# Optimization experiments

Measured on AMD Instinct MI355X. Metric: run time of the kernel, lower is better.

The kernel has to match this reference:

```python
import jax, jax.numpy as jnp
import numpy as np
from jax import lax

INPUT_DIM = 256
STATE_DIM = 512
B, T = 128, 1024


def setup_inputs() -> dict:
    key = jax.random.key(0)
    ks = jax.random.split(key, 9)
    s = STATE_DIM
    i = INPUT_DIM
    # Linear(state_dim, state_dim, bias=False), weight scaled by 0.2 as in __init__
    lim_s = 1.0 / np.sqrt(s)
    lim_i = 1.0 / np.sqrt(i)
    A0_w = jax.random.uniform(ks[0], (s, s), jnp.float32, -lim_s, lim_s) * 0.2
    A1_w = jax.random.uniform(ks[1], (s, s), jnp.float32, -lim_s, lim_s) * 0.2
    B0_w = jax.random.uniform(ks[2], (s, i), jnp.float32, -lim_i, lim_i)
    B0_b = jax.random.uniform(ks[3], (s,), jnp.float32, -lim_i, lim_i)
    B1_w = jax.random.uniform(ks[4], (s, i), jnp.float32, -lim_i, lim_i)
    B1_b = jax.random.uniform(ks[5], (s,), jnp.float32, -lim_i, lim_i)
    gate_w = jax.random.uniform(ks[6], (s, i), jnp.float32, -lim_i, lim_i)
    gate_b = jax.random.uniform(ks[7], (s,), jnp.float32, -lim_i, lim_i)
    x_seq = jax.random.normal(ks[8], (B, T, i), jnp.float32)
    s0 = jnp.zeros((B, s), jnp.float32)
    alpha = jnp.float32(0.5)
    return {
        "x_seq": x_seq, "s0": s0,
        "A0_w": A0_w, "B0_w": B0_w, "B0_b": B0_b,
        "A1_w": A1_w, "B1_w": B1_w, "B1_b": B1_b,
        "gate_w": gate_w, "gate_b": gate_b,
        "alpha": alpha, "z": 1,
    }


def reference(x_seq, s0, A0_w, B0_w, B0_b, A1_w, B1_w, B1_b, gate_w, gate_b, alpha, z):
    # Precompute all input projections in one batched GEMM each: [B, T, S]
    bx0 = jnp.einsum('bti,si->bts', x_seq, B0_w) + B0_b
    bx1 = jnp.einsum('bti,si->bts', x_seq, B1_w) + B1_b
    gx = jax.nn.sigmoid(jnp.einsum('bti,si->bts', x_seq, gate_w) + gate_b)

    def step_fn(s, inputs):
        b0_t, b1_t, g_t = inputs  # each [B, S]
        f0 = jnp.tanh(s @ A0_w.T + b0_t)
        if z == 0:
            f = f0
        else:
            f1 = jnp.tanh(s @ A1_w.T + b1_t)
            f = (1.0 - alpha) * f0 + alpha * f1
        s_new = g_t * f + (1.0 - g_t) * s
        return s_new, s_new

    # scan over time: move T to leading axis
    xs = (jnp.swapaxes(bx0, 0, 1), jnp.swapaxes(bx1, 0, 1), jnp.swapaxes(gx, 0, 1))
    _, states = lax.scan(step_fn, s0, xs)  # states: [T, B, S]
    # prepend s0 -> [B, T+1, S]
    return jnp.concatenate([s0[:, None, :], jnp.swapaxes(states, 0, 1)], axis=1)
```

## Files before the change

### kernel.cpp

```cpp
#include <hip/hip_runtime.h>
#include <hip/hip_bf16.h>
#include <math.h>

typedef __attribute__((ext_vector_type(8))) short bf16x8;
typedef __attribute__((ext_vector_type(4))) float f32x4;
typedef __attribute__((ext_vector_type(4))) unsigned int u32x4;
typedef __attribute__((ext_vector_type(2))) unsigned int u32x2;

#define TT 1024
#define BB 128
#define II 256
#define SS 512
#define OUT_T 1025
#define OUT_BSTRIDE ((size_t)OUT_T * SS)

static __device__ __forceinline__ unsigned short f2bf(float f) {
  union { float f; unsigned int u; } v; v.f = f;
  unsigned int r = v.u + 0x7fffu + ((v.u >> 16) & 1u);
  return (unsigned short)(r >> 16);
}
static __device__ __forceinline__ float bf2f(unsigned short h) {
  union { unsigned int u; float f; } v; v.u = ((unsigned int)h) << 16;
  return v.f;
}
static __device__ __forceinline__ bf16x8 pack8(const float* p) {
  float4 a = *(const float4*)p;
  float4 b = *(const float4*)(p + 4);
  bf16x8 r;
  r[0]=(short)f2bf(a.x); r[1]=(short)f2bf(a.y); r[2]=(short)f2bf(a.z); r[3]=(short)f2bf(a.w);
  r[4]=(short)f2bf(b.x); r[5]=(short)f2bf(b.y); r[6]=(short)f2bf(b.z); r[7]=(short)f2bf(b.w);
  return r;
}
static __device__ __forceinline__ float bfat(u32x2 v, int q) {
  unsigned int u = (q < 2) ? v[0] : v[1];
  u = (q & 1) ? (u >> 16) : (u & 0xffffu);
  return bf2f((unsigned short)u);
}
static __device__ __forceinline__ float fast_tanh(float x) {
  float x2 = fminf(x * 2.8853900817779268f, 88.0f);
  float e = __builtin_amdgcn_exp2f(x2);
  return (e - 1.0f) * __builtin_amdgcn_rcpf(e + 1.0f);
}

static __device__ __forceinline__ void st_coh_b128(void* p, u32x4 v) {
  asm volatile("global_store_dwordx4 %0, %1, off sc0 sc1" :: "v"(p), "v"(v) : "memory");
}

static __device__ __forceinline__ void mega_acquire(const char* an,
    u32x4& v0, u32x4& v1, u32x4& v2, u32x4& v3,
    u32x4& v4, u32x4& v5, u32x4& v6, u32x4& v7) {
  asm volatile(
    "global_load_dwordx4 %0, %8, off sc0 sc1\n\t"
    "global_load_dwordx4 %1, %8, off offset:256 sc0 sc1\n\t"
    "global_load_dwordx4 %2, %8, off offset:512 sc0 sc1\n\t"
    "global_load_dwordx4 %3, %8, off offset:768 sc0 sc1\n\t"
    "global_load_dwordx4 %4, %8, off offset:1024 sc0 sc1\n\t"
    "global_load_dwordx4 %5, %8, off offset:1280 sc0 sc1\n\t"
    "global_load_dwordx4 %6, %8, off offset:1536 sc0 sc1\n\t"
    "global_load_dwordx4 %7, %8, off offset:1792 sc0 sc1\n\t"
    "s_waitcnt vmcnt(0)"
    : "=&v"(v0), "=&v"(v1), "=&v"(v2), "=&v"(v3),
      "=&v"(v4), "=&v"(v5), "=&v"(v6), "=&v"(v7)
    : "v"(an) : "memory");
  __builtin_amdgcn_sched_barrier(0);
}
static __device__ __forceinline__ unsigned chk4(u32x4 v, unsigned expd) {
  return ((((v[0] ^ expd) | (v[1] ^ expd) | (v[2] ^ expd) | (v[3] ^ expd)) & 0xffffu) != 0u) ? 1u : 0u;
}

__global__ __launch_bounds__(256) void proj_kernel(
    const float* __restrict__ x,
    const float* __restrict__ B0w, const float* __restrict__ B0b,
    const float* __restrict__ B1w, const float* __restrict__ B1b,
    const float* __restrict__ Gw,  const float* __restrict__ Gb,
    unsigned short* __restrict__ proj)
{
  __shared__ unsigned short Xs[64 * 264];
  __shared__ unsigned short Ws[64 * 40];

  int m0 = blockIdx.x * 64;
  int tid = threadIdx.x, lane = tid & 63, wid = tid >> 6;
  int lane15 = lane & 15, kslot = lane >> 4;
  int mt0 = (wid >> 1) * 2, nt0 = (wid & 1) * 2;
  int sr = tid >> 2, sc = tid & 3;

#pragma unroll
  for (int it = 0; it < 8; ++it) {
    int task = tid + 256 * it; int r = task >> 5, c = task & 31;
    *(bf16x8*)&Xs[r * 264 + c * 8] = pack8(x + (size_t)(m0 + r) * II + c * 8);
  }
  __syncthreads();

  for (int nt = 0; nt < 24; ++nt) {
    int n0 = nt * 64;
    const float* Wp; const float* bp; bool isgate = false;
    if (n0 < 512)       { Wp = B0w + (size_t)n0 * II;          bp = B0b + n0; }
    else if (n0 < 1024) { Wp = B1w + (size_t)(n0 - 512) * II;  bp = B1b + (n0 - 512); }
    else                { Wp = Gw  + (size_t)(n0 - 1024) * II; bp = Gb + (n0 - 1024); isgate = true; }

    f32x4 acc[2][2] = {};
    for (int k0 = 0; k0 < II; k0 += 32) {
      __syncthreads();
      *(bf16x8*)&Ws[sr * 40 + sc * 8] = pack8(Wp + (size_t)sr * II + k0 + sc * 8);
      __syncthreads();
      bf16x8 af[2], bf[2];
#pragma unroll
      for (int mi = 0; mi < 2; ++mi)
        af[mi] = *(const bf16x8*)&Xs[((mt0 + mi) * 16 + lane15) * 264 + k0 + 8 * kslot];
#pragma unroll
      for (int ni = 0; ni < 2; ++ni)
        bf[ni] = *(const bf16x8*)&Ws[((nt0 + ni) * 16 + lane15) * 40 + 8 * kslot];
#pragma unroll
      for (int mi = 0; mi < 2; ++mi)
#pragma unroll
        for (int ni = 0; ni < 2; ++ni)
          acc[mi][ni] = __builtin_amdgcn_mfma_f32_16x16x32_bf16(af[mi], bf[ni], acc[mi][ni], 0, 0, 0);
    }
#pragma unroll
    for (int mi = 0; mi < 2; ++mi)
#pragma unroll
      for (int ni = 0; ni < 2; ++ni)
#pragma unroll
        for (int q = 0; q < 4; ++q) {
          int m  = m0 + (mt0 + mi) * 16 + kslot * 4 + q;
          int nl = (nt0 + ni) * 16 + lane15;
          int b = m >> 10, t = m & 1023;
          float v = acc[mi][ni][q] + bp[nl];
          if (isgate) v = 1.0f / (1.0f + expf(-v));
          proj[((size_t)t * BB + b) * 1536 + n0 + nl] = f2bf(v);
        }
  }
}

__global__ __launch_bounds__(256, 1) void recur_kernel(
    const float* __restrict__ s0,
    const float* __restrict__ A0w, const float* __restrict__ A1w,
    const unsigned short* __restrict__ proj,
    const float* __restrict__ alpha_p, const int* __restrict__ z_p,
    unsigned int* state32,
    float* __restrict__ out)
{
  __shared__ unsigned short Sbuf[2][16 * 520];

  int tid = threadIdx.x, lane = tid & 63, wid = tid >> 6;
  int g = blockIdx.x & 7, j = blockIdx.x >> 3;
  int b0 = g * 16, c0 = j * 64;
  int lane15 = lane & 15, kslot = lane >> 4;
  int colA = c0 + wid * 16 + lane15;
  int ccb  = c0 + wid * 16 + kslot * 4;
  int row  = b0 + lane15;
  int prow = tid >> 4, pch = tid & 15;
  float alpha = *alpha_p; int z = *z_p; float om_a = 1.0f - alpha;

  bf16x8 Af0[16], Af1[16];
#pragma unroll
  for (int kk = 0; kk < 16; ++kk) {
    int k0 = kk * 32 + kslot * 8;
    Af0[kk] = pack8(A0w + (size_t)colA * SS + k0);
    Af1[kk] = pack8(A1w + (size_t)colA * SS + k0);
  }

#pragma unroll
  for (int c2 = 0; c2 < 4; ++c2) {
    int e = tid + 256 * c2; int rr = e >> 6, kc = e & 63;
    *(bf16x8*)&Sbuf[0][rr * 520 + kc * 8] = pack8(s0 + (size_t)(b0 + rr) * SS + kc * 8);
  }
  if (j == 0) {
#pragma unroll
    for (int it = 0; it < 8; ++it) {
      int task = tid + 256 * it;
      int rr = task >> 7, f4 = task & 127;
      *(float4*)(out + (size_t)(b0 + rr) * OUT_BSTRIDE + f4 * 4) =
          *(const float4*)(s0 + (size_t)(b0 + rr) * SS + f4 * 4);
    }
  }
  float4 sp4 = *(const float4*)(s0 + (size_t)row * SS + ccb);
  float sprev[4] = {sp4.x, sp4.y, sp4.z, sp4.w};

  const unsigned short* pp = proj + (size_t)row * 1536 + ccb;
  u32x2 pb0 = *(const u32x2*)(pp);
  u32x2 pb1 = *(const u32x2*)(pp + 512);
  u32x2 pg  = *(const u32x2*)(pp + 1024);

  unsigned int* pub0 = state32 + (size_t)row * SS + ccb;
  unsigned int* pub1 = pub0 + (size_t)BB * SS;
  const char* acq0 = (const char*)(state32 + (size_t)(b0 + prow) * SS) + pch * 16;
  const char* acq1 = acq0 + (size_t)BB * SS * 4;
  float* outp = out + (size_t)row * OUT_BSTRIDE + ccb;

  __syncthreads();

  for (int t = 0; t < TT; ++t) {
    int par = t & 1;

    if (t > 0) {
      unsigned expd = (unsigned)t;
      const char* acqc = par ? acq1 : acq0;
      u32x4 v0, v1, v2, v3, v4, v5, v6, v7;
      mega_acquire(acqc, v0, v1, v2, v3, v4, v5, v6, v7);
      unsigned own = 1u << j;
      for (;;) {
        unsigned st =
            (chk4(v0, expd) << 0) | (chk4(v1, expd) << 1) |
            (chk4(v2, expd) << 2) | (chk4(v3, expd) << 3) |
            (chk4(v4, expd) << 4) | (chk4(v5, expd) << 5) |
            (chk4(v6, expd) << 6) | (chk4(v7, expd) << 7);
        st &= ~own;
        if (st == 0u) break;
        mega_acquire(acqc, v0, v1, v2, v3, v4, v5, v6, v7);
      }
      unsigned short* sl = &Sbuf[par][prow * 520 + pch * 4];
#define LAND(S, V) if ((S) != j) {                                    \
        unsigned d0 = ((V)[0] >> 16) | ((V)[1] & 0xffff0000u);        \
        unsigned d1 = ((V)[2] >> 16) | ((V)[3] & 0xffff0000u);        \
        u32x2 dd; dd[0] = d0; dd[1] = d1;                             \
        *(u32x2*)(sl + (S) * 64) = dd; }
      LAND(0, v0) LAND(1, v1) LAND(2, v2) LAND(3, v3)
      LAND(4, v4) LAND(5, v5) LAND(6, v6) LAND(7, v7)
#undef LAND
      __syncthreads();
    }

    f32x4 a0e = {}, a0o = {}, a1e = {}, a1o = {};
    const unsigned short* sb = &Sbuf[par][lane15 * 520 + kslot * 8];
#pragma unroll
    for (int kk = 0; kk < 16; kk += 2) {
      bf16x8 f0 = *(const bf16x8*)(sb + kk * 32);
      bf16x8 f1 = *(const bf16x8*)(sb + (kk + 1) * 32);
      a0e = __builtin_amdgcn_mfma_f32_16x16x32_bf16(Af0[kk],     f0, a0e, 0, 0, 0);
      a1e = __builtin_amdgcn_mfma_f32_16x16x32_bf16(Af1[kk],     f0, a1e, 0, 0, 0);
      a0o = __builtin_amdgcn_mfma_f32_16x16x32_bf16(Af0[kk + 1], f1, a0o, 0, 0, 0);
      a1o = __builtin_amdgcn_mfma_f32_16x16x32_bf16(Af1[kk + 1], f1, a1o, 0, 0, 0);
    }

    float sn[4];
#pragma unroll
    for (int q = 0; q < 4; ++q) {
      float f0 = fast_tanh((a0e[q] + a0o[q]) + bfat(pb0, q));
      float f;
      if (z != 0) {
        float f1 = fast_tanh((a1e[q] + a1o[q]) + bfat(pb1, q));
        f = om_a * f0 + alpha * f1;
      } else f = f0;
      float gg = bfat(pg, q);
      sn[q] = gg * f + (1.0f - gg) * sprev[q];
      sprev[q] = sn[q];
    }

    {
      u32x2 dd;
      dd[0] = (unsigned)f2bf(sn[0]) | ((unsigned)f2bf(sn[1]) << 16);
      dd[1] = (unsigned)f2bf(sn[2]) | ((unsigned)f2bf(sn[3]) << 16);
      *(u32x2*)&Sbuf[par ^ 1][lane15 * 520 + ccb] = dd;
    }
    {
      unsigned nxt = (unsigned)(t + 1);
      u32x4 w;
#pragma unroll
      for (int q = 0; q < 4; ++q) w[q] = ((unsigned)f2bf(sn[q]) << 16) | nxt;
      st_coh_b128(par ? pub0 : pub1, w);
    }
    outp += SS;
    {
      float4 o4 = {sn[0], sn[1], sn[2], sn[3]};
      *(float4*)outp = o4;
    }
    if (t + 1 < TT) {
      pp += (size_t)BB * 1536;
      pb0 = *(const u32x2*)(pp);
      pb1 = *(const u32x2*)(pp + 512);
      pg  = *(const u32x2*)(pp + 1024);
    }
  }
}

extern "C" void kernel_launch(void* const* d_in, const int* in_sizes, int n_in,
                              void* d_out, int out_size, void* d_ws, size_t ws_size,
                              hipStream_t stream) {
  const float* x   = (const float*)d_in[0];
  const float* s0  = (const float*)d_in[1];
  const float* A0w = (const float*)d_in[2];
  const float* B0w = (const float*)d_in[3];
  const float* B0b = (const float*)d_in[4];
  const float* A1w = (const float*)d_in[5];
  const float* B1w = (const float*)d_in[6];
  const float* B1b = (const float*)d_in[7];
  const float* Gw  = (const float*)d_in[8];
  const float* Gb  = (const float*)d_in[9];
  const float* alp = (const float*)d_in[10];
  const int*   zp  = (const int*)d_in[11];
  float* out = (float*)d_out;

  char* ws = (char*)d_ws;
  size_t proj_bytes  = (size_t)BB * TT * 1536 * 2;
  size_t state_bytes = (size_t)2 * BB * SS * 4;
  unsigned short* proj    = (unsigned short*)(ws);
  unsigned int*   state32 = (unsigned int*)(ws + proj_bytes);

  hipMemsetAsync(state32, 0, state_bytes, stream);

  proj_kernel<<<dim3(131072 / 64), dim3(256), 0, stream>>>(
      x, B0w, B0b, B1w, B1b, Gw, Gb, proj);

  recur_kernel<<<dim3(64), dim3(256), 0, stream>>>(
      s0, A0w, A1w, proj, alp, zp, state32, out);
}
```

Baseline: 3.031 ms.

## Interleave two batch groups per block to hide inter-block state exchange latency

The recurrence kernel now runs on 32 blocks instead of 64, and each block handles two 16-row batch groups (A and B). Per time step it alternates: acquire A's state, compute and publish A, then acquire B's state and compute B. The goal is for one group's cross-block exchange latency to overlap with the other group's MFMA and tanh work. Each group uses a single LDS buffer, and the block's own slice is now read back through the global exchange rather than written locally. The cost is that each block does twice the serial work per step, and fewer CUs are in use.

```diff
diff --git a/kernel.cpp b/kernel.cpp
--- a/kernel.cpp
+++ b/kernel.cpp
@@ -46,7 +46,7 @@
   asm volatile("global_store_dwordx4 %0, %1, off sc0 sc1" :: "v"(p), "v"(v) : "memory");
 }
 
-static __device__ __forceinline__ void mega_acquire(const char* an,
+static __device__ __forceinline__ void mega_acq(const char* an,
     u32x4& v0, u32x4& v1, u32x4& v2, u32x4& v3,
     u32x4& v4, u32x4& v5, u32x4& v6, u32x4& v7) {
   asm volatile(
@@ -140,15 +140,17 @@
     unsigned int* state32,
     float* __restrict__ out)
 {
-  __shared__ unsigned short Sbuf[2][16 * 520];
+  __shared__ unsigned short SbufA[16 * 520];
+  __shared__ unsigned short SbufB[16 * 520];
 
   int tid = threadIdx.x, lane = tid & 63, wid = tid >> 6;
-  int g = blockIdx.x & 7, j = blockIdx.x >> 3;
-  int b0 = g * 16, c0 = j * 64;
+  int gg = blockIdx.x & 3, j = blockIdx.x >> 2;
+  int bA = gg * 32, bB = gg * 32 + 16;
+  int c0 = j * 64;
   int lane15 = lane & 15, kslot = lane >> 4;
   int colA = c0 + wid * 16 + lane15;
   int ccb  = c0 + wid * 16 + kslot * 4;
-  int row  = b0 + lane15;
+  int rowA = bA + lane15, rowB = bB + lane15;
   int prow = tid >> 4, pch = tid & 15;
   float alpha = *alpha_p; int z = *z_p; float om_a = 1.0f - alpha;
 
@@ -163,115 +165,181 @@
 #pragma unroll
   for (int c2 = 0; c2 < 4; ++c2) {
     int e = tid + 256 * c2; int rr = e >> 6, kc = e & 63;
-    *(bf16x8*)&Sbuf[0][rr * 520 + kc * 8] = pack8(s0 + (size_t)(b0 + rr) * SS + kc * 8);
+    *(bf16x8*)&SbufA[rr * 520 + kc * 8] = pack8(s0 + (size_t)(bA + rr) * SS + kc * 8);
+    *(bf16x8*)&SbufB[rr * 520 + kc * 8] = pack8(s0 + (size_t)(bB + rr) * SS + kc * 8);
   }
   if (j == 0) {
 #pragma unroll
-    for (int it = 0; it < 8; ++it) {
+    for (int it = 0; it < 16; ++it) {
       int task = tid + 256 * it;
       int rr = task >> 7, f4 = task & 127;
-      *(float4*)(out + (size_t)(b0 + rr) * OUT_BSTRIDE + f4 * 4) =
-          *(const float4*)(s0 + (size_t)(b0 + rr) * SS + f4 * 4);
-    }
-  }
-  float4 sp4 = *(const float4*)(s0 + (size_t)row * SS + ccb);
-  float sprev[4] = {sp4.x, sp4.y, sp4.z, sp4.w};
-
-  const unsigned short* pp = proj + (size_t)row * 1536 + ccb;
-  u32x2 pb0 = *(const u32x2*)(pp);
-  u32x2 pb1 = *(const u32x2*)(pp + 512);
-  u32x2 pg  = *(const u32x2*)(pp + 1024);
-
-  unsigned int* pub0 = state32 + (size_t)row * SS + ccb;
-  unsigned int* pub1 = pub0 + (size_t)BB * SS;
-  const char* acq0 = (const char*)(state32 + (size_t)(b0 + prow) * SS) + pch * 16;
-  const char* acq1 = acq0 + (size_t)BB * SS * 4;
-  float* outp = out + (size_t)row * OUT_BSTRIDE + ccb;
+      *(float4*)(out + (size_t)(bA + rr) * OUT_BSTRIDE + f4 * 4) =
+          *(const float4*)(s0 + (size_t)(bA + rr) * SS + f4 * 4);
+    }
+  }
+  float4 sA4 = *(const float4*)(s0 + (size_t)rowA * SS + ccb);
+  float4 sB4 = *(const float4*)(s0 + (size_t)rowB * SS + ccb);
+  float sprevA[4] = {sA4.x, sA4.y, sA4.z, sA4.w};
+  float sprevB[4] = {sB4.x, sB4.y, sB4.z, sB4.w};
+
+  const unsigned short* ppA = proj + (size_t)rowA * 1536 + ccb;
+  const unsigned short* ppB = proj + (size_t)rowB * 1536 + ccb;
+  u32x2 pA0 = *(const u32x2*)(ppA), pA1 = *(const u32x2*)(ppA + 512), pAg = *(const u32x2*)(ppA + 1024);
+  u32x2 pB0 = *(const u32x2*)(ppB), pB1 = *(const u32x2*)(ppB + 512), pBg = *(const u32x2*)(ppB + 1024);
+
+  unsigned int* pubA0 = state32 + (size_t)rowA * SS + ccb;
+  unsigned int* pubA1 = pubA0 + (size_t)BB * SS;
+  unsigned int* pubB0 = state32 + (size_t)rowB * SS + ccb;
+  unsigned int* pubB1 = pubB0 + (size_t)BB * SS;
+  const char* acqA0 = (const char*)(state32 + (size_t)(bA + prow) * SS) + pch * 16;
+  const char* acqA1 = acqA0 + (size_t)BB * SS * 4;
+  const char* acqB0 = (const char*)(state32 + (size_t)(bB + prow) * SS) + pch * 16;
+  const char* acqB1 = acqB0 + (size_t)BB * SS * 4;
+  float* outA = out + (size_t)rowA * OUT_BSTRIDE + ccb;
+  float* outB = out + (size_t)rowB * OUT_BSTRIDE + ccb;
 
   __syncthreads();
+
+#define LANDALL(SL, V0,V1,V2,V3,V4,V5,V6,V7) do {                      \
+    unsigned short* sl_ = (SL) + prow * 520 + pch * 4;                 \
+    u32x2 dd_;                                                         \
+    dd_[0] = ((V0)[0] >> 16) | ((V0)[1] & 0xffff0000u);                \
+    dd_[1] = ((V0)[2] >> 16) | ((V0)[3] & 0xffff0000u);                \
+    *(u32x2*)(sl_ + 0 * 64) = dd_;                                     \
+    dd_[0] = ((V1)[0] >> 16) | ((V1)[1] & 0xffff0000u);                \
+    dd_[1] = ((V1)[2] >> 16) | ((V1)[3] & 0xffff0000u);                \
+    *(u32x2*)(sl_ + 1 * 64) = dd_;                                     \
+    dd_[0] = ((V2)[0] >> 16) | ((V2)[1] & 0xffff0000u);                \
+    dd_[1] = ((V2)[2] >> 16) | ((V2)[3] & 0xffff0000u);                \
+    *(u32x2*)(sl_ + 2 * 64) = dd_;                                     \
+    dd_[0] = ((V3)[0] >> 16) | ((V3)[1] & 0xffff0000u);                \
+    dd_[1] = ((V3)[2] >> 16) | ((V3)[3] & 0xffff0000u);                \
+    *(u32x2*)(sl_ + 3 * 64) = dd_;                                     \
+    dd_[0] = ((V4)[0] >> 16) | ((V4)[1] & 0xffff0000u);                \
+    dd_[1] = ((V4)[2] >> 16) | ((V4)[3] & 0xffff0000u);                \
+    *(u32x2*)(sl_ + 4 * 64) = dd_;                                     \
+    dd_[0] = ((V5)[0] >> 16) | ((V5)[1] & 0xffff0000u);                \
+    dd_[1] = ((V5)[2] >> 16) | ((V5)[3] & 0xffff0000u);                \
+    *(u32x2*)(sl_ + 5 * 64) = dd_;                                     \
+    dd_[0] = ((V6)[0] >> 16) | ((V6)[1] & 0xffff0000u);                \
+    dd_[1] = ((V6)[2] >> 16) | ((V6)[3] & 0xffff0000u);                \
+    *(u32x2*)(sl_ + 6 * 64) = dd_;                                     \
+    dd_[0] = ((V7)[0] >> 16) | ((V7)[1] & 0xffff0000u);                \
+    dd_[1] = ((V7)[2] >> 16) | ((V7)[3] & 0xffff0000u);                \
+    *(u32x2*)(sl_ + 7 * 64) = dd_;                                     \
+  } while (0)
 
   for (int t = 0; t < TT; ++t) {
     int par = t & 1;
+    unsigned expd = (unsigned)t;
 
     if (t > 0) {
-      unsigned expd = (unsigned)t;
-      const char* acqc = par ? acq1 : acq0;
+      const char* an = par ? acqA1 : acqA0;
       u32x4 v0, v1, v2, v3, v4, v5, v6, v7;
-      mega_acquire(acqc, v0, v1, v2, v3, v4, v5, v6, v7);
-      unsigned own = 1u << j;
-      for (;;) {
-        unsigned st =
-            (chk4(v0, expd) << 0) | (chk4(v1, expd) << 1) |
-            (chk4(v2, expd) << 2) | (chk4(v3, expd) << 3) |
-            (chk4(v4, expd) << 4) | (chk4(v5, expd) << 5) |
-            (chk4(v6, expd) << 6) | (chk4(v7, expd) << 7);
-        st &= ~own;
-        if (st == 0u) break;
-        mega_acquire(acqc, v0, v1, v2, v3, v4, v5, v6, v7);
-      }
-      unsigned short* sl = &Sbuf[par][prow * 520 + pch * 4];
-#define LAND(S, V) if ((S) != j) {                                    \
-        unsigned d0 = ((V)[0] >> 16) | ((V)[1] & 0xffff0000u);        \
-        unsigned d1 = ((V)[2] >> 16) | ((V)[3] & 0xffff0000u);        \
-        u32x2 dd; dd[0] = d0; dd[1] = d1;                             \
-        *(u32x2*)(sl + (S) * 64) = dd; }
-      LAND(0, v0) LAND(1, v1) LAND(2, v2) LAND(3, v3)
-      LAND(4, v4) LAND(5, v5) LAND(6, v6) LAND(7, v7)
-#undef LAND
-      __syncthreads();
-    }
-
-    f32x4 a0e = {}, a0o = {}, a1e = {}, a1o = {};
-    const unsigned short* sb = &Sbuf[par][lane15 * 520 + kslot * 8];
-#pragma unroll
-    for (int kk = 0; kk < 16; kk += 2) {
-      bf16x8 f0 = *(const bf16x8*)(sb + kk * 32);
-      bf16x8 f1 = *(const bf16x8*)(sb + (kk + 1) * 32);
-      a0e = __builtin_amdgcn_mfma_f32_16x16x32_bf16(Af0[kk],     f0, a0e, 0, 0, 0);
-      a1e = __builtin_amdgcn_mfma_f32_16x16x32_bf16(Af1[kk],     f0, a1e, 0, 0, 0);
-      a0o = __builtin_amdgcn_mfma_f32_16x16x32_bf16(Af0[kk + 1], f1, a0o, 0, 0, 0);
-      a1o = __builtin_amdgcn_mfma_f32_16x16x32_bf16(Af1[kk + 1], f1, a1o, 0, 0, 0);
-    }
-
-    float sn[4];
-#pragma unroll
-    for (int q = 0; q < 4; ++q) {
-      float f0 = fast_tanh((a0e[q] + a0o[q]) + bfat(pb0, q));
-      float f;
-      if (z != 0) {
-        float f1 = fast_tanh((a1e[q] + a1o[q]) + bfat(pb1, q));
-        f = om_a * f0 + alpha * f1;
-      } else f = f0;
-      float gg = bfat(pg, q);
-      sn[q] = gg * f + (1.0f - gg) * sprev[q];
-      sprev[q] = sn[q];
-    }
+      mega_acq(an, v0, v1, v2, v3, v4, v5, v6, v7);
+      while ((chk4(v0, expd) | chk4(v1, expd) | chk4(v2, expd) | chk4(v3, expd) |
+              chk4(v4, expd) | chk4(v5, expd) | chk4(v6, expd) | chk4(v7, expd)) != 0u)
+        mega_acq(an, v0, v1, v2, v3, v4, v5, v6, v7);
+      LANDALL(SbufA, v0, v1, v2, v3, v4, v5, v6, v7);
+    }
+    __syncthreads();
 
     {
-      u32x2 dd;
-      dd[0] = (unsigned)f2bf(sn[0]) | ((unsigned)f2bf(sn[1]) << 16);
-      dd[1] = (unsigned)f2bf(sn[2]) | ((unsigned)f2bf(sn[3]) << 16);
-      *(u32x2*)&Sbuf[par ^ 1][lane15 * 520 + ccb] = dd;
-    }
+      f32x4 a0e = {}, a0o = {}, a1e = {}, a1o = {};
+      const unsigned short* sb = &SbufA[lane15 * 520 + kslot * 8];
+#pragma unroll
+      for (int kk = 0; kk < 16; kk += 2) {
+        bf16x8 f0 = *(const bf16x8*)(sb + kk * 32);
+        bf16x8 f1 = *(const bf16x8*)(sb + (kk + 1) * 32);
+        a0e = __builtin_amdgcn_mfma_f32_16x16x32_bf16(Af0[kk],     f0, a0e, 0, 0, 0);
+        a1e = __builtin_amdgcn_mfma_f32_16x16x32_bf16(Af1[kk],     f0, a1e, 0, 0, 0);
+        a0o = __builtin_amdgcn_mfma_f32_16x16x32_bf16(Af0[kk + 1], f1, a0o, 0, 0, 0);
+        a1o = __builtin_amdgcn_mfma_f32_16x16x32_bf16(Af1[kk + 1], f1, a1o, 0, 0, 0);
+      }
+      float sn[4];
+#pragma unroll
+      for (int q = 0; q < 4; ++q) {
+        float f0 = fast_tanh((a0e[q] + a0o[q]) + bfat(pA0, q));
+        float f;
+        if (z != 0) {
+          float f1 = fast_tanh((a1e[q] + a1o[q]) + bfat(pA1, q));
+          f = om_a * f0 + alpha * f1;
+        } else f = f0;
+        float gval = bfat(pAg, q);
+        sn[q] = gval * f + (1.0f - gval) * sprevA[q];
+        sprevA[q] = sn[q];
+      }
+      {
+        unsigned nxt = (unsigned)(t + 1);
+        u32x4 w;
+#pragma unroll
+        for (int q = 0; q < 4; ++q) w[q] = ((unsigned)f2bf(sn[q]) << 16) | nxt;
+        st_coh_b128(par ? pubA0 : pubA1, w);
+      }
+      outA += SS;
+      { float4 o4 = {sn[0], sn[1], sn[2], sn[3]}; *(float4*)outA = o4; }
+      if (t + 1 < TT) {
+        ppA += (size_t)BB * 1536;
+        pA0 = *(const u32x2*)(ppA);
+        pA1 = *(const u32x2*)(ppA + 512);
+        pAg = *(const u32x2*)(ppA + 1024);
+      }
+    }
+
+    if (t > 0) {
+      const char* an = par ? acqB1 : acqB0;
+      u32x4 v0, v1, v2, v3, v4, v5, v6, v7;
+      mega_acq(an, v0, v1, v2, v3, v4, v5, v6, v7);
+      while ((chk4(v0, expd) | chk4(v1, expd) | chk4(v2, expd) | chk4(v3, expd) |
+              chk4(v4, expd) | chk4(v5, expd) | chk4(v6, expd) | chk4(v7, expd)) != 0u)
+        mega_acq(an, v0, v1, v2, v3, v4, v5, v6, v7);
+      LANDALL(SbufB, v0, v1, v2, v3, v4, v5, v6, v7);
+    }
+    __syncthreads();
+
     {
-      unsigned nxt = (unsigned)(t + 1);
-      u32x4 w;
-#pragma unroll
-      for (int q = 0; q < 4; ++q) w[q] = ((unsigned)f2bf(sn[q]) << 16) | nxt;
-      st_coh_b128(par ? pub0 : pub1, w);
-    }
-    outp += SS;
-    {
-      float4 o4 = {sn[0], sn[1], sn[2], sn[3]};
-      *(float4*)outp = o4;
-    }
-    if (t + 1 < TT) {
-      pp += (size_t)BB * 1536;
-      pb0 = *(const u32x2*)(pp);
-      pb1 = *(const u32x2*)(pp + 512);
-      pg  = *(const u32x2*)(pp + 1024);
-    }
-  }
+      f32x4 a0e = {}, a0o = {}, a1e = {}, a1o = {};
+      const unsigned short* sb = &SbufB[lane15 * 520 + kslot * 8];
+#pragma unroll
+      for (int kk = 0; kk < 16; kk += 2) {
+        bf16x8 f0 = *(const bf16x8*)(sb + kk * 32);
+        bf16x8 f1 = *(const bf16x8*)(sb + (kk + 1) * 32);
+        a0e = __builtin_amdgcn_mfma_f32_16x16x32_bf16(Af0[kk],     f0, a0e, 0, 0, 0);
+        a1e = __builtin_amdgcn_mfma_f32_16x16x32_bf16(Af1[kk],     f0, a1e, 0, 0, 0);
+        a0o = __builtin_amdgcn_mfma_f32_16x16x32_bf16(Af0[kk + 1], f1, a0o, 0, 0, 0);
+        a1o = __builtin_amdgcn_mfma_f32_16x16x32_bf16(Af1[kk + 1], f1, a1o, 0, 0, 0);
+      }
+      float sn[4];
+#pragma unroll
+      for (int q = 0; q < 4; ++q) {
+        float f0 = fast_tanh((a0e[q] + a0o[q]) + bfat(pB0, q));
+        float f;
+        if (z != 0) {
+          float f1 = fast_tanh((a1e[q] + a1o[q]) + bfat(pB1, q));
+          f = om_a * f0 + alpha * f1;
+        } else f = f0;
+        float gval = bfat(pBg, q);
+        sn[q] = gval * f + (1.0f - gval) * sprevB[q];
+        sprevB[q] = sn[q];
+      }
+      {
+        unsigned nxt = (unsigned)(t + 1);
+        u32x4 w;
+#pragma unroll
+        for (int q = 0; q < 4; ++q) w[q] = ((unsigned)f2bf(sn[q]) << 16) | nxt;
+        st_coh_b128(par ? pubB0 : pubB1, w);
+      }
+      outB += SS;
+      { float4 o4 = {sn[0], sn[1], sn[2], sn[3]}; *(float4*)outB = o4; }
+      if (t + 1 < TT) {
+        ppB += (size_t)BB * 1536;
+        pB0 = *(const u32x2*)(ppB);
+        pB1 = *(const u32x2*)(ppB + 512);
+        pBg = *(const u32x2*)(ppB + 1024);
+      }
+    }
+  }
+#undef LANDALL
 }
 
 extern "C" void kernel_launch(void* const* d_in, const int* in_sizes, int n_in,
@@ -302,6 +370,6 @@
   proj_kernel<<<dim3(131072 / 64), dim3(256), 0, stream>>>(
       x, B0w, B0b, B1w, B1b, Gw, Gb, proj);
 
-  recur_kernel<<<dim3(64), dim3(256), 0, stream>>>(
+  recur_kernel<<<dim3(32), dim3(256), 0, stream>>>(
       s0, A0w, A1w, proj, alp, zp, state32, out);
 }
```

Measured after the change: 4.919 ms. 62.3% more time.
